# Optimization experiments

Hardware: AMD Instinct MI355X
Metric: run time of the kernel (lower is better)

The kernel has to match this reference:

```python
import jax, jax.numpy as jnp
from jax import lax
import numpy as np

B, T, IN, H = 8192, 512, 5, 32


def setup_inputs() -> dict:
    key = jax.random.key(0)
    ks = jax.random.split(key, 7)
    s_ih = 1.0 / np.sqrt(H)
    return {
        "x": jax.random.normal(ks[0], (B, T, IN), dtype=jnp.float32),
        "W_ih": jax.random.normal(ks[1], (4 * H, IN), dtype=jnp.float32) * s_ih,
        "W_hh": jax.random.normal(ks[2], (4 * H, H), dtype=jnp.float32) * s_ih,
        "b_ih": jax.random.normal(ks[3], (4 * H,), dtype=jnp.float32) * s_ih,
        "b_hh": jax.random.normal(ks[4], (4 * H,), dtype=jnp.float32) * s_ih,
        "W_fc": jax.random.normal(ks[5], (1, H), dtype=jnp.float32) * s_ih,
        "b_fc": jax.random.normal(ks[6], (1,), dtype=jnp.float32) * s_ih,
    }


def reference(x, W_ih, W_hh, b_ih, b_hh, W_fc, b_fc):
    # x: [B, T, IN]. Single-layer batch-first LSTM (PyTorch gate order i,f,g,o),
    # then linear head on the final timestep's hidden state.
    b = x.shape[0]
    h0 = jnp.zeros((b, H), x.dtype)
    c0 = jnp.zeros((b, H), x.dtype)
    # Precompute input projections for all timesteps in one GEMM: [T, B, 4H]
    x_t = jnp.swapaxes(x, 0, 1)  # [T, B, IN]
    x_proj = jnp.einsum("tbi,gi->tbg", x_t, W_ih) + b_ih + b_hh

    def step(carry, xp):
        h, c = carry
        gates = xp + h @ W_hh.T  # [B, 4H]
        i, f, g, o = jnp.split(gates, 4, axis=-1)
        i = jax.nn.sigmoid(i)
        f = jax.nn.sigmoid(f)
        g = jnp.tanh(g)
        o = jax.nn.sigmoid(o)
        c = f * c + i * g
        h = o * jnp.tanh(c)
        return (h, c), None

    (h_last, _), _ = lax.scan(step, (h0, c0), x_proj)
    return h_last @ W_fc.T + b_fc  # [B, 1]
```

## Files before the change

kernel.cpp:

```cpp
#include <hip/hip_runtime.h>


typedef __attribute__((ext_vector_type(8))) short short8;
typedef __attribute__((ext_vector_type(4))) float f32x4;
typedef __attribute__((ext_vector_type(4))) unsigned int u32x4;

static constexpr int BB  = 8192;
static constexpr int TT  = 512;
static constexpr int NIN = 5;
static constexpr int HH  = 32;

__device__ __forceinline__ unsigned short bf_rne(float f) {
    unsigned int u = __float_as_uint(f);
    u = (u + 0x7FFFu + ((u >> 16) & 1u)) >> 16;
    return (unsigned short)u;
}
__device__ __forceinline__ float bf_f32(unsigned short h) {
    return __uint_as_float((unsigned int)h << 16);
}
__device__ __forceinline__ float fast_sigmoid(float x) {
    float e = __builtin_amdgcn_exp2f(-1.4426950408889634f * x);
    return __builtin_amdgcn_rcpf(1.0f + e);
}
__device__ __forceinline__ float fast_tanh(float x) {
    float e = __builtin_amdgcn_exp2f(2.8853900817779268f * x);
    return 1.0f - 2.0f * __builtin_amdgcn_rcpf(1.0f + e);
}

__global__ __launch_bounds__(64) void lstm_wave(
    const float* __restrict__ x,
    const float* __restrict__ W_ih,
    const float* __restrict__ W_hh,
    const float* __restrict__ b_ih,
    const float* __restrict__ b_hh,
    const float* __restrict__ W_fc,
    const float* __restrict__ b_fc,
    float* __restrict__ out)
{
    const int lane = threadIdx.x & 63;
    const int col  = lane & 15;
    const int kg   = lane >> 4;
    const int b0   = blockIdx.x * 8;
    const int bloc = col & 7;
    const bool jlow = (col < 8);
    const int jbase = 4 * kg + (jlow ? 0 : 16);

    short8 Ahh_hi[8], Ahh_lo[8], Ax[8];
#pragma unroll
    for (int t4 = 0; t4 < 8; ++t4) {
        const int gr = 16 * t4 + col;
#pragma unroll
        for (int e = 0; e < 8; ++e) {
            float wv = W_hh[gr * HH + kg * 8 + e];
            unsigned short hi = bf_rne(wv);
            Ahh_hi[t4][e] = (short)hi;
            Ahh_lo[t4][e] = (short)bf_rne(wv - bf_f32(hi));
        }
        float bias = b_ih[gr] + b_hh[gr];
        unsigned short bh_ = bf_rne(bias);
        unsigned short bl_ = bf_rne(bias - bf_f32(bh_));
        short8 v;
#pragma unroll
        for (int e = 0; e < 8; ++e) v[e] = 0;
        if (kg == 0 || kg == 1) {
#pragma unroll
            for (int e = 0; e < NIN; ++e) v[e] = (short)bf_rne(W_ih[gr * NIN + e]);
            v[5] = (short)((kg == 0) ? bh_ : bl_);
        } else if (kg == 2) {
#pragma unroll
            for (int e = 0; e < NIN; ++e) {
                float wv = W_ih[gr * NIN + e];
                unsigned short h2 = bf_rne(wv);
                v[e] = (short)bf_rne(wv - bf_f32(h2));
            }
        }
        Ax[t4] = v;
    }

    const int xb = (lane / 5 < 8) ? (lane / 5) : 7;
    int xe = lane - 5 * xb; if (xe > 4) xe = 4;
    const float* px = x + ((size_t)(b0 + xb) * TT) * NIN + xe;

    const unsigned shx  = (kg == 1) ? 16u : 0u;
    const unsigned mskx = (kg == 3) ? 0u : 0xFFFFu;
    const unsigned one5 = (kg < 2) ? (0x3F80u << 16) : 0u;

    const int srcA = 32 * (kg & 1) + bloc + 8 * (kg >> 1);
    const int srcB = srcA + 16;

    float xv = px[0]; px += NIN;
    unsigned int xpk = 0;
    {
        unsigned short hi = bf_rne(xv);
        unsigned short lo = bf_rne(xv - bf_f32(hi));
        xpk = (unsigned int)hi | ((unsigned int)lo << 16);
    }

    unsigned int bh0 = 0, bh1 = 0, bh2 = 0, bh3 = 0;
    float c0 = 0.f, c1 = 0.f, c2 = 0.f, c3 = 0.f;
    float h0 = 0.f, h1 = 0.f, h2 = 0.f, h3 = 0.f;

    const f32x4 z = {0.f, 0.f, 0.f, 0.f};

#pragma unroll 1
    for (int t = 0; t < TT; ++t) {
        float xvn = xv;
        if (t + 1 < TT) { xvn = px[0]; px += NIN; }

        unsigned int p0x = (unsigned)__shfl((int)xpk, 5 * bloc + 0, 64);
        unsigned int p1x = (unsigned)__shfl((int)xpk, 5 * bloc + 1, 64);
        unsigned int p2x = (unsigned)__shfl((int)xpk, 5 * bloc + 2, 64);
        unsigned int p3x = (unsigned)__shfl((int)xpk, 5 * bloc + 3, 64);
        unsigned int p4x = (unsigned)__shfl((int)xpk, 5 * bloc + 4, 64);
        unsigned int a0 = (p0x >> shx) & mskx;
        unsigned int a1 = (p1x >> shx) & mskx;
        unsigned int a2 = (p2x >> shx) & mskx;
        unsigned int a3 = (p3x >> shx) & mskx;
        unsigned int a4 = (p4x >> shx) & mskx;
        u32x4 bxu = {a0 | (a1 << 16), a2 | (a3 << 16), a4 | one5, 0u};
        short8 bx = __builtin_bit_cast(short8, bxu);
        u32x4 bhu = {bh0, bh1, bh2, bh3};
        short8 bh = __builtin_bit_cast(short8, bhu);

        f32x4 acc[8];
#pragma unroll
        for (int t4 = 0; t4 < 8; ++t4)
            acc[t4] = __builtin_amdgcn_mfma_f32_16x16x32_bf16(Ahh_lo[t4], bh, z, 0, 0, 0);
#pragma unroll
        for (int t4 = 0; t4 < 8; ++t4)
            acc[t4] = __builtin_amdgcn_mfma_f32_16x16x32_bf16(Ahh_hi[t4], bh, acc[t4], 0, 0, 0);
#pragma unroll
        for (int t4 = 0; t4 < 8; ++t4)
            acc[t4] = __builtin_amdgcn_mfma_f32_16x16x32_bf16(Ax[t4], bx, acc[t4], 0, 0, 0);

#pragma unroll
        for (int r = 0; r < 4; ++r) {
            float gi = jlow ? acc[0][r] : acc[1][r];
            float gf = jlow ? acc[2][r] : acc[3][r];
            float gg = jlow ? acc[4][r] : acc[5][r];
            float go = jlow ? acc[6][r] : acc[7][r];
            float iv = fast_sigmoid(gi);
            float fv = fast_sigmoid(gf);
            float gv = fast_tanh(gg);
            float ov = fast_sigmoid(go);
            float cc = (r == 0 ? c0 : r == 1 ? c1 : r == 2 ? c2 : c3);
            cc = fv * cc + iv * gv;
            float hh = ov * fast_tanh(cc);
            if (r == 0) { c0 = cc; h0 = hh; }
            else if (r == 1) { c1 = cc; h1 = hh; }
            else if (r == 2) { c2 = cc; h2 = hh; }
            else { c3 = cc; h3 = hh; }
        }

        unsigned int p0 = (unsigned int)bf_rne(h0) | ((unsigned int)bf_rne(h1) << 16);
        unsigned int p1 = (unsigned int)bf_rne(h2) | ((unsigned int)bf_rne(h3) << 16);
        bh0 = (unsigned)__shfl((int)p0, srcA, 64);
        bh1 = (unsigned)__shfl((int)p1, srcA, 64);
        bh2 = (unsigned)__shfl((int)p0, srcB, 64);
        bh3 = (unsigned)__shfl((int)p1, srcB, 64);

        {
            unsigned short hi = bf_rne(xvn);
            unsigned short lo = bf_rne(xvn - bf_f32(hi));
            xpk = (unsigned int)hi | ((unsigned int)lo << 16);
        }
        xv = xvn;
    }

    float v = h0 * W_fc[jbase + 0] + h1 * W_fc[jbase + 1]
            + h2 * W_fc[jbase + 2] + h3 * W_fc[jbase + 3];
    v += __shfl_xor(v, 8);
    v += __shfl_xor(v, 16);
    v += __shfl_xor(v, 32);
    if (lane < 8) out[b0 + lane] = v + b_fc[0];
}

extern "C" void kernel_launch(void* const* d_in, const int* in_sizes, int n_in,
                              void* d_out, int out_size, void* d_ws, size_t ws_size,
                              hipStream_t stream) {
    const float* x    = (const float*)d_in[0];
    const float* W_ih = (const float*)d_in[1];
    const float* W_hh = (const float*)d_in[2];
    const float* b_ih = (const float*)d_in[3];
    const float* b_hh = (const float*)d_in[4];
    const float* W_fc = (const float*)d_in[5];
    const float* b_fc = (const float*)d_in[6];
    float* out = (float*)d_out;

    lstm_wave<<<dim3(BB / 8), dim3(64), 0, stream>>>(
        x, W_ih, W_hh, b_ih, b_hh, W_fc, b_fc, out);
}
```

Baseline: 330.2 us.

## Process four batch rows per wave to halve per-lane gate math

Each wave now handles 4 batch rows instead of 8, so every lane evaluates 2 LSTM cells per step rather than 4, and the grid doubles to 2048 waves. The shuffle mapping for the recurrent hidden state is rebuilt for the new column layout, and hardware packed bf16 conversion replaces the manual round-to-nearest code. This shortens the serial per-step activation chain. The cost is that the MFMA work per step stays the same while half of each MFMA's columns are redundant, so total matrix work doubles. A launch-bounds occupancy hint is added too.

```diff
diff --git a/kernel.cpp b/kernel.cpp
--- a/kernel.cpp
+++ b/kernel.cpp
@@ -26,8 +26,13 @@
     float e = __builtin_amdgcn_exp2f(2.8853900817779268f * x);
     return 1.0f - 2.0f * __builtin_amdgcn_rcpf(1.0f + e);
 }
-
-__global__ __launch_bounds__(64) void lstm_wave(
+__device__ __forceinline__ unsigned int cvt_pk_bf16(float a, float b) {
+    unsigned int r;
+    asm("v_cvt_pk_bf16_f32 %0, %1, %2" : "=v"(r) : "v"(a), "v"(b));
+    return r;
+}
+
+__global__ __launch_bounds__(64, 2) void lstm_wave4(
     const float* __restrict__ x,
     const float* __restrict__ W_ih,
     const float* __restrict__ W_hh,
@@ -37,13 +42,15 @@
     const float* __restrict__ b_fc,
     float* __restrict__ out)
 {
-    const int lane = threadIdx.x & 63;
-    const int col  = lane & 15;
-    const int kg   = lane >> 4;
-    const int b0   = blockIdx.x * 8;
-    const int bloc = col & 7;
-    const bool jlow = (col < 8);
-    const int jbase = 4 * kg + (jlow ? 0 : 16);
+    const int lane  = threadIdx.x & 63;
+    const int col   = lane & 15;
+    const int kg    = lane >> 4;
+    const int bloc  = col & 3;
+    const int cq    = col >> 2;
+    const int jhigh = cq >> 1;
+    const int rp    = cq & 1;
+    const int b0    = blockIdx.x * 4;
+    const int j0    = 16 * jhigh + 4 * kg + 2 * rp;
 
     short8 Ahh_hi[8], Ahh_lo[8], Ax[8];
 #pragma unroll
@@ -77,29 +84,38 @@
         Ax[t4] = v;
     }
 
-    const int xb = (lane / 5 < 8) ? (lane / 5) : 7;
+    const int xb = (lane / 5 < 4) ? (lane / 5) : 3;
     int xe = lane - 5 * xb; if (xe > 4) xe = 4;
     const float* px = x + ((size_t)(b0 + xb) * TT) * NIN + xe;
 
     const unsigned shx  = (kg == 1) ? 16u : 0u;
-    const unsigned mskx = (kg == 3) ? 0u : 0xFFFFu;
     const unsigned one5 = (kg < 2) ? (0x3F80u << 16) : 0u;
 
-    const int srcA = 32 * (kg & 1) + bloc + 8 * (kg >> 1);
-    const int srcB = srcA + 16;
+    int src0, src1, src2, src3;
+    {
+        int s[4];
+#pragma unroll
+        for (int w = 0; w < 4; ++w) {
+            const int j0s = 8 * kg + 2 * w;
+            const int jhs = j0s >> 4;
+            const int rem = j0s & 15;
+            const int kgs = rem >> 2;
+            const int rps = (rem >> 1) & 1;
+            s[w] = 16 * kgs + 4 * (2 * jhs + rps) + bloc;
+        }
+        src0 = s[0]; src1 = s[1]; src2 = s[2]; src3 = s[3];
+    }
 
     float xv = px[0]; px += NIN;
-    unsigned int xpk = 0;
+    unsigned int xpk;
     {
-        unsigned short hi = bf_rne(xv);
-        unsigned short lo = bf_rne(xv - bf_f32(hi));
-        xpk = (unsigned int)hi | ((unsigned int)lo << 16);
+        unsigned int t0 = cvt_pk_bf16(xv, xv);
+        float hif = __uint_as_float(t0 << 16);
+        xpk = cvt_pk_bf16(xv, xv - hif);
     }
 
     unsigned int bh0 = 0, bh1 = 0, bh2 = 0, bh3 = 0;
-    float c0 = 0.f, c1 = 0.f, c2 = 0.f, c3 = 0.f;
-    float h0 = 0.f, h1 = 0.f, h2 = 0.f, h3 = 0.f;
-
+    float cA = 0.f, cB = 0.f, hA = 0.f, hB = 0.f;
     const f32x4 z = {0.f, 0.f, 0.f, 0.f};
 
 #pragma unroll 1
@@ -112,11 +128,11 @@
         unsigned int p2x = (unsigned)__shfl((int)xpk, 5 * bloc + 2, 64);
         unsigned int p3x = (unsigned)__shfl((int)xpk, 5 * bloc + 3, 64);
         unsigned int p4x = (unsigned)__shfl((int)xpk, 5 * bloc + 4, 64);
-        unsigned int a0 = (p0x >> shx) & mskx;
-        unsigned int a1 = (p1x >> shx) & mskx;
-        unsigned int a2 = (p2x >> shx) & mskx;
-        unsigned int a3 = (p3x >> shx) & mskx;
-        unsigned int a4 = (p4x >> shx) & mskx;
+        unsigned int a0 = (p0x >> shx) & 0xFFFFu;
+        unsigned int a1 = (p1x >> shx) & 0xFFFFu;
+        unsigned int a2 = (p2x >> shx) & 0xFFFFu;
+        unsigned int a3 = (p3x >> shx) & 0xFFFFu;
+        unsigned int a4 = (p4x >> shx) & 0xFFFFu;
         u32x4 bxu = {a0 | (a1 << 16), a2 | (a3 << 16), a4 | one5, 0u};
         short8 bx = __builtin_bit_cast(short8, bxu);
         u32x4 bhu = {bh0, bh1, bh2, bh3};
@@ -133,46 +149,52 @@
         for (int t4 = 0; t4 < 8; ++t4)
             acc[t4] = __builtin_amdgcn_mfma_f32_16x16x32_bf16(Ax[t4], bx, acc[t4], 0, 0, 0);
 
-#pragma unroll
-        for (int r = 0; r < 4; ++r) {
-            float gi = jlow ? acc[0][r] : acc[1][r];
-            float gf = jlow ? acc[2][r] : acc[3][r];
-            float gg = jlow ? acc[4][r] : acc[5][r];
-            float go = jlow ? acc[6][r] : acc[7][r];
-            float iv = fast_sigmoid(gi);
-            float fv = fast_sigmoid(gf);
-            float gv = fast_tanh(gg);
-            float ov = fast_sigmoid(go);
-            float cc = (r == 0 ? c0 : r == 1 ? c1 : r == 2 ? c2 : c3);
-            cc = fv * cc + iv * gv;
-            float hh = ov * fast_tanh(cc);
-            if (r == 0) { c0 = cc; h0 = hh; }
-            else if (r == 1) { c1 = cc; h1 = hh; }
-            else if (r == 2) { c2 = cc; h2 = hh; }
-            else { c3 = cc; h3 = hh; }
-        }
-
-        unsigned int p0 = (unsigned int)bf_rne(h0) | ((unsigned int)bf_rne(h1) << 16);
-        unsigned int p1 = (unsigned int)bf_rne(h2) | ((unsigned int)bf_rne(h3) << 16);
-        bh0 = (unsigned)__shfl((int)p0, srcA, 64);
-        bh1 = (unsigned)__shfl((int)p1, srcA, 64);
-        bh2 = (unsigned)__shfl((int)p0, srcB, 64);
-        bh3 = (unsigned)__shfl((int)p1, srcB, 64);
+        float giA = jhigh ? (rp ? acc[1][2] : acc[1][0]) : (rp ? acc[0][2] : acc[0][0]);
+        float gfA = jhigh ? (rp ? acc[3][2] : acc[3][0]) : (rp ? acc[2][2] : acc[2][0]);
+        float ggA = jhigh ? (rp ? acc[5][2] : acc[5][0]) : (rp ? acc[4][2] : acc[4][0]);
+        float goA = jhigh ? (rp ? acc[7][2] : acc[7][0]) : (rp ? acc[6][2] : acc[6][0]);
+        float giB = jhigh ? (rp ? acc[1][3] : acc[1][1]) : (rp ? acc[0][3] : acc[0][1]);
+        float gfB = jhigh ? (rp ? acc[3][3] : acc[3][1]) : (rp ? acc[2][3] : acc[2][1]);
+        float ggB = jhigh ? (rp ? acc[5][3] : acc[5][1]) : (rp ? acc[4][3] : acc[4][1]);
+        float goB = jhigh ? (rp ? acc[7][3] : acc[7][1]) : (rp ? acc[6][3] : acc[6][1]);
 
         {
-            unsigned short hi = bf_rne(xvn);
-            unsigned short lo = bf_rne(xvn - bf_f32(hi));
-            xpk = (unsigned int)hi | ((unsigned int)lo << 16);
+            float iv = fast_sigmoid(giA);
+            float fv = fast_sigmoid(gfA);
+            float gv = fast_tanh(ggA);
+            float ov = fast_sigmoid(goA);
+            cA = fv * cA + iv * gv;
+            hA = ov * fast_tanh(cA);
+        }
+        {
+            float iv = fast_sigmoid(giB);
+            float fv = fast_sigmoid(gfB);
+            float gv = fast_tanh(ggB);
+            float ov = fast_sigmoid(goB);
+            cB = fv * cB + iv * gv;
+            hB = ov * fast_tanh(cB);
+        }
+
+        unsigned int p = cvt_pk_bf16(hA, hB);
+        bh0 = (unsigned)__shfl((int)p, src0, 64);
+        bh1 = (unsigned)__shfl((int)p, src1, 64);
+        bh2 = (unsigned)__shfl((int)p, src2, 64);
+        bh3 = (unsigned)__shfl((int)p, src3, 64);
+
+        {
+            unsigned int t0 = cvt_pk_bf16(xvn, xvn);
+            float hif = __uint_as_float(t0 << 16);
+            xpk = cvt_pk_bf16(xvn, xvn - hif);
         }
         xv = xvn;
     }
 
-    float v = h0 * W_fc[jbase + 0] + h1 * W_fc[jbase + 1]
-            + h2 * W_fc[jbase + 2] + h3 * W_fc[jbase + 3];
+    float v = hA * W_fc[j0] + hB * W_fc[j0 + 1];
+    v += __shfl_xor(v, 4);
     v += __shfl_xor(v, 8);
     v += __shfl_xor(v, 16);
     v += __shfl_xor(v, 32);
-    if (lane < 8) out[b0 + lane] = v + b_fc[0];
+    if (lane < 4) out[b0 + lane] = v + b_fc[0];
 }
 
 extern "C" void kernel_launch(void* const* d_in, const int* in_sizes, int n_in,
@@ -187,6 +209,6 @@
     const float* b_fc = (const float*)d_in[6];
     float* out = (float*)d_out;
 
-    lstm_wave<<<dim3(BB / 8), dim3(64), 0, stream>>>(
+    lstm_wave4<<<dim3(BB / 4), dim3(64), 0, stream>>>(
         x, W_ih, W_hh, b_ih, b_hh, W_fc, b_fc, out);
 }
```

Result: slower. 366.2 us (+10.9%).

## Split each wave's batch into two independent MFMA chains for ILP

Applied to the files above, without the earlier changes.

Each wave still handles 8 batch rows, but they now form two groups of 4, each with its own MFMA accumulator chain, so the two recurrences can interleave and hide MFMA and transcendental latency. The lane-to-column mapping and the hidden-state shuffle pattern are reworked so each lane owns 2 hidden units per group, which halves the per-lane gate nonlinearity work. Sigmoid pairs share one reciprocal, bf16 packing uses v_cvt_pk_bf16_f32, and each lane loads its x inputs directly instead of shuffling them. The cost is twice the MFMA count per step (16-column tiles are half empty) and higher register pressure.

```diff
diff --git a/kernel.cpp b/kernel.cpp
--- a/kernel.cpp
+++ b/kernel.cpp
@@ -9,6 +9,8 @@
 static constexpr int TT  = 512;
 static constexpr int NIN = 5;
 static constexpr int HH  = 32;
+static constexpr float K1 = 1.4426950408889634f;
+static constexpr float K2 = 2.8853900817779268f;
 
 __device__ __forceinline__ unsigned short bf_rne(float f) {
     unsigned int u = __float_as_uint(f);
@@ -18,16 +20,13 @@
 __device__ __forceinline__ float bf_f32(unsigned short h) {
     return __uint_as_float((unsigned int)h << 16);
 }
-__device__ __forceinline__ float fast_sigmoid(float x) {
-    float e = __builtin_amdgcn_exp2f(-1.4426950408889634f * x);
-    return __builtin_amdgcn_rcpf(1.0f + e);
-}
-__device__ __forceinline__ float fast_tanh(float x) {
-    float e = __builtin_amdgcn_exp2f(2.8853900817779268f * x);
-    return 1.0f - 2.0f * __builtin_amdgcn_rcpf(1.0f + e);
-}
-
-__global__ __launch_bounds__(64) void lstm_wave(
+__device__ __forceinline__ unsigned int cvt_pk_bf16(float a, float b) {
+    unsigned int r;
+    asm("v_cvt_pk_bf16_f32 %0, %1, %2" : "=v"(r) : "v"(a), "v"(b));
+    return r;
+}
+
+__global__ __launch_bounds__(64, 1) void lstm_ilp2(
     const float* __restrict__ x,
     const float* __restrict__ W_ih,
     const float* __restrict__ W_hh,
@@ -40,10 +39,12 @@
     const int lane = threadIdx.x & 63;
     const int col  = lane & 15;
     const int kg   = lane >> 4;
+    const int bloc = col & 3;
+    const int q    = col >> 2;
+    const bool jsel = (q & 1);
+    const bool rp   = (q >> 1);
     const int b0   = blockIdx.x * 8;
-    const int bloc = col & 7;
-    const bool jlow = (col < 8);
-    const int jbase = 4 * kg + (jlow ? 0 : 16);
+    const int j0   = 16 * (q & 1) + 4 * kg + 2 * (q >> 1);
 
     short8 Ahh_hi[8], Ahh_lo[8], Ax[8];
 #pragma unroll
@@ -77,102 +78,161 @@
         Ax[t4] = v;
     }
 
-    const int xb = (lane / 5 < 8) ? (lane / 5) : 7;
-    int xe = lane - 5 * xb; if (xe > 4) xe = 4;
-    const float* px = x + ((size_t)(b0 + xb) * TT) * NIN + xe;
-
-    const unsigned shx  = (kg == 1) ? 16u : 0u;
-    const unsigned mskx = (kg == 3) ? 0u : 0xFFFFu;
-    const unsigned one5 = (kg < 2) ? (0x3F80u << 16) : 0u;
-
-    const int srcA = 32 * (kg & 1) + bloc + 8 * (kg >> 1);
-    const int srcB = srcA + 16;
-
-    float xv = px[0]; px += NIN;
-    unsigned int xpk = 0;
+    int src0, src1, src2, src3;
     {
-        unsigned short hi = bf_rne(xv);
-        unsigned short lo = bf_rne(xv - bf_f32(hi));
-        xpk = (unsigned int)hi | ((unsigned int)lo << 16);
-    }
-
-    unsigned int bh0 = 0, bh1 = 0, bh2 = 0, bh3 = 0;
-    float c0 = 0.f, c1 = 0.f, c2 = 0.f, c3 = 0.f;
-    float h0 = 0.f, h1 = 0.f, h2 = 0.f, h3 = 0.f;
-
+        int s[4];
+#pragma unroll
+        for (int m = 0; m < 4; ++m) {
+            const int jw  = 8 * kg + 2 * m;
+            const int kgo = (jw & 15) >> 2;
+            const int qp  = (jw >> 4) + 2 * ((jw >> 1) & 1);
+            s[m] = 16 * kgo + 4 * qp + bloc;
+        }
+        src0 = s[0]; src1 = s[1]; src2 = s[2]; src3 = s[3];
+    }
+
+    const unsigned mskAll = (kg == 3) ? 0u : 0xFFFFFFFFu;
+    const unsigned msk45  = (kg == 3) ? 0u : ((kg == 2) ? 0x0000FFFFu : 0xFFFFFFFFu);
+    const bool isLo = (kg == 1);
+
+    const float* pA = x + (size_t)(b0 + bloc) * TT * NIN;
+    const float* pB = x + (size_t)(b0 + 4 + bloc) * TT * NIN;
+    float xA[NIN], xB[NIN];
+#pragma unroll
+    for (int e = 0; e < NIN; ++e) { xA[e] = pA[e]; xB[e] = pB[e]; }
+
+    unsigned int bhA0 = 0, bhA1 = 0, bhA2 = 0, bhA3 = 0;
+    unsigned int bhB0 = 0, bhB1 = 0, bhB2 = 0, bhB3 = 0;
+    float cA0 = 0.f, cA1 = 0.f, cB0 = 0.f, cB1 = 0.f;
+    float hA0 = 0.f, hA1 = 0.f, hB0 = 0.f, hB1 = 0.f;
     const f32x4 z = {0.f, 0.f, 0.f, 0.f};
+
+    auto make_bx = [&](const float* xv) -> short8 {
+        unsigned H01 = cvt_pk_bf16(xv[0], xv[1]);
+        unsigned H23 = cvt_pk_bf16(xv[2], xv[3]);
+        unsigned H45 = cvt_pk_bf16(xv[4], 1.0f);
+        float l0 = xv[0] - __uint_as_float(H01 << 16);
+        float l1 = xv[1] - __uint_as_float(H01 & 0xFFFF0000u);
+        float l2 = xv[2] - __uint_as_float(H23 << 16);
+        float l3 = xv[3] - __uint_as_float(H23 & 0xFFFF0000u);
+        float l4 = xv[4] - __uint_as_float(H45 << 16);
+        unsigned L01 = cvt_pk_bf16(l0, l1);
+        unsigned L23 = cvt_pk_bf16(l2, l3);
+        unsigned L45 = cvt_pk_bf16(l4, 1.0f);
+        unsigned w0 = (isLo ? L01 : H01) & mskAll;
+        unsigned w1 = (isLo ? L23 : H23) & mskAll;
+        unsigned w2 = (isLo ? L45 : H45) & msk45;
+        u32x4 u = {w0, w1, w2, 0u};
+        return __builtin_bit_cast(short8, u);
+    };
+
+    auto cell = [&](float gi, float gf, float gg, float go, float& c) -> float {
+        float ea = __builtin_amdgcn_exp2f(-K1 * gi);
+        float eb = __builtin_amdgcn_exp2f(-K1 * gf);
+        float u = 1.f + ea, v = 1.f + eb;
+        float r = __builtin_amdgcn_rcpf(u * v);
+        float iv = v * r, fv = u * r;
+        float eg = __builtin_amdgcn_exp2f(K2 * gg);
+        float eo = __builtin_amdgcn_exp2f(-K1 * go);
+        float u2 = 1.f + eg, v2 = 1.f + eo;
+        float r2 = __builtin_amdgcn_rcpf(u2 * v2);
+        float gv = 1.f - 2.f * (v2 * r2);
+        float ov = u2 * r2;
+        c = fmaf(fv, c, iv * gv);
+        float et = __builtin_amdgcn_exp2f(K2 * c);
+        float tc = 1.f - 2.f * __builtin_amdgcn_rcpf(1.f + et);
+        return ov * tc;
+    };
 
 #pragma unroll 1
     for (int t = 0; t < TT; ++t) {
-        float xvn = xv;
-        if (t + 1 < TT) { xvn = px[0]; px += NIN; }
-
-        unsigned int p0x = (unsigned)__shfl((int)xpk, 5 * bloc + 0, 64);
-        unsigned int p1x = (unsigned)__shfl((int)xpk, 5 * bloc + 1, 64);
-        unsigned int p2x = (unsigned)__shfl((int)xpk, 5 * bloc + 2, 64);
-        unsigned int p3x = (unsigned)__shfl((int)xpk, 5 * bloc + 3, 64);
-        unsigned int p4x = (unsigned)__shfl((int)xpk, 5 * bloc + 4, 64);
-        unsigned int a0 = (p0x >> shx) & mskx;
-        unsigned int a1 = (p1x >> shx) & mskx;
-        unsigned int a2 = (p2x >> shx) & mskx;
-        unsigned int a3 = (p3x >> shx) & mskx;
-        unsigned int a4 = (p4x >> shx) & mskx;
-        u32x4 bxu = {a0 | (a1 << 16), a2 | (a3 << 16), a4 | one5, 0u};
-        short8 bx = __builtin_bit_cast(short8, bxu);
-        u32x4 bhu = {bh0, bh1, bh2, bh3};
-        short8 bh = __builtin_bit_cast(short8, bhu);
-
-        f32x4 acc[8];
-#pragma unroll
-        for (int t4 = 0; t4 < 8; ++t4)
-            acc[t4] = __builtin_amdgcn_mfma_f32_16x16x32_bf16(Ahh_lo[t4], bh, z, 0, 0, 0);
-#pragma unroll
-        for (int t4 = 0; t4 < 8; ++t4)
-            acc[t4] = __builtin_amdgcn_mfma_f32_16x16x32_bf16(Ahh_hi[t4], bh, acc[t4], 0, 0, 0);
-#pragma unroll
-        for (int t4 = 0; t4 < 8; ++t4)
-            acc[t4] = __builtin_amdgcn_mfma_f32_16x16x32_bf16(Ax[t4], bx, acc[t4], 0, 0, 0);
-
-#pragma unroll
-        for (int r = 0; r < 4; ++r) {
-            float gi = jlow ? acc[0][r] : acc[1][r];
-            float gf = jlow ? acc[2][r] : acc[3][r];
-            float gg = jlow ? acc[4][r] : acc[5][r];
-            float go = jlow ? acc[6][r] : acc[7][r];
-            float iv = fast_sigmoid(gi);
-            float fv = fast_sigmoid(gf);
-            float gv = fast_tanh(gg);
-            float ov = fast_sigmoid(go);
-            float cc = (r == 0 ? c0 : r == 1 ? c1 : r == 2 ? c2 : c3);
-            cc = fv * cc + iv * gv;
-            float hh = ov * fast_tanh(cc);
-            if (r == 0) { c0 = cc; h0 = hh; }
-            else if (r == 1) { c1 = cc; h1 = hh; }
-            else if (r == 2) { c2 = cc; h2 = hh; }
-            else { c3 = cc; h3 = hh; }
-        }
-
-        unsigned int p0 = (unsigned int)bf_rne(h0) | ((unsigned int)bf_rne(h1) << 16);
-        unsigned int p1 = (unsigned int)bf_rne(h2) | ((unsigned int)bf_rne(h3) << 16);
-        bh0 = (unsigned)__shfl((int)p0, srcA, 64);
-        bh1 = (unsigned)__shfl((int)p1, srcA, 64);
-        bh2 = (unsigned)__shfl((int)p0, srcB, 64);
-        bh3 = (unsigned)__shfl((int)p1, srcB, 64);
+        const size_t off = (size_t)((t + 1 < TT) ? (t + 1) : t) * NIN;
+        float nA[NIN], nB[NIN];
+#pragma unroll
+        for (int e = 0; e < NIN; ++e) { nA[e] = pA[off + e]; nB[e] = pB[off + e]; }
+
+        short8 bxA = make_bx(xA);
+        short8 bxB = make_bx(xB);
+        u32x4 ua = {bhA0, bhA1, bhA2, bhA3};
+        u32x4 ub = {bhB0, bhB1, bhB2, bhB3};
+        short8 bhA = __builtin_bit_cast(short8, ua);
+        short8 bhB = __builtin_bit_cast(short8, ub);
+
+        f32x4 aA[8], aB[8];
+#pragma unroll
+        for (int t4 = 0; t4 < 8; ++t4) {
+            aA[t4] = __builtin_amdgcn_mfma_f32_16x16x32_bf16(Ahh_lo[t4], bhA, z, 0, 0, 0);
+            aB[t4] = __builtin_amdgcn_mfma_f32_16x16x32_bf16(Ahh_lo[t4], bhB, z, 0, 0, 0);
+        }
+#pragma unroll
+        for (int t4 = 0; t4 < 8; ++t4) {
+            aA[t4] = __builtin_amdgcn_mfma_f32_16x16x32_bf16(Ahh_hi[t4], bhA, aA[t4], 0, 0, 0);
+            aB[t4] = __builtin_amdgcn_mfma_f32_16x16x32_bf16(Ahh_hi[t4], bhB, aB[t4], 0, 0, 0);
+        }
+#pragma unroll
+        for (int t4 = 0; t4 < 8; ++t4) {
+            aA[t4] = __builtin_amdgcn_mfma_f32_16x16x32_bf16(Ax[t4], bxA, aA[t4], 0, 0, 0);
+            aB[t4] = __builtin_amdgcn_mfma_f32_16x16x32_bf16(Ax[t4], bxB, aB[t4], 0, 0, 0);
+        }
 
         {
-            unsigned short hi = bf_rne(xvn);
-            unsigned short lo = bf_rne(xvn - bf_f32(hi));
-            xpk = (unsigned int)hi | ((unsigned int)lo << 16);
-        }
-        xv = xvn;
-    }
-
-    float v = h0 * W_fc[jbase + 0] + h1 * W_fc[jbase + 1]
-            + h2 * W_fc[jbase + 2] + h3 * W_fc[jbase + 3];
-    v += __shfl_xor(v, 8);
-    v += __shfl_xor(v, 16);
-    v += __shfl_xor(v, 32);
-    if (lane < 8) out[b0 + lane] = v + b_fc[0];
+            float g[4][2];
+#pragma unroll
+            for (int G = 0; G < 4; ++G) {
+                f32x4 tA = aA[2 * G], tB = aA[2 * G + 1];
+                float s0 = jsel ? tB[0] : tA[0];
+                float s1 = jsel ? tB[1] : tA[1];
+                float s2 = jsel ? tB[2] : tA[2];
+                float s3 = jsel ? tB[3] : tA[3];
+                g[G][0] = rp ? s2 : s0;
+                g[G][1] = rp ? s3 : s1;
+            }
+            hA0 = cell(g[0][0], g[1][0], g[2][0], g[3][0], cA0);
+            hA1 = cell(g[0][1], g[1][1], g[2][1], g[3][1], cA1);
+        }
+        {
+            float g[4][2];
+#pragma unroll
+            for (int G = 0; G < 4; ++G) {
+                f32x4 tA = aB[2 * G], tB = aB[2 * G + 1];
+                float s0 = jsel ? tB[0] : tA[0];
+                float s1 = jsel ? tB[1] : tA[1];
+                float s2 = jsel ? tB[2] : tA[2];
+                float s3 = jsel ? tB[3] : tA[3];
+                g[G][0] = rp ? s2 : s0;
+                g[G][1] = rp ? s3 : s1;
+            }
+            hB0 = cell(g[0][0], g[1][0], g[2][0], g[3][0], cB0);
+            hB1 = cell(g[0][1], g[1][1], g[2][1], g[3][1], cB1);
+        }
+
+        unsigned int pkA = cvt_pk_bf16(hA0, hA1);
+        unsigned int pkB = cvt_pk_bf16(hB0, hB1);
+        bhA0 = (unsigned)__shfl((int)pkA, src0, 64);
+        bhA1 = (unsigned)__shfl((int)pkA, src1, 64);
+        bhA2 = (unsigned)__shfl((int)pkA, src2, 64);
+        bhA3 = (unsigned)__shfl((int)pkA, src3, 64);
+        bhB0 = (unsigned)__shfl((int)pkB, src0, 64);
+        bhB1 = (unsigned)__shfl((int)pkB, src1, 64);
+        bhB2 = (unsigned)__shfl((int)pkB, src2, 64);
+        bhB3 = (unsigned)__shfl((int)pkB, src3, 64);
+
+#pragma unroll
+        for (int e = 0; e < NIN; ++e) { xA[e] = nA[e]; xB[e] = nB[e]; }
+    }
+
+    const float w0 = W_fc[j0], w1 = W_fc[j0 + 1];
+    float vA = hA0 * w0 + hA1 * w1;
+    float vB = hB0 * w0 + hB1 * w1;
+    vA += __shfl_xor(vA, 4);  vB += __shfl_xor(vB, 4);
+    vA += __shfl_xor(vA, 8);  vB += __shfl_xor(vB, 8);
+    vA += __shfl_xor(vA, 16); vB += __shfl_xor(vB, 16);
+    vA += __shfl_xor(vA, 32); vB += __shfl_xor(vB, 32);
+    if (lane < 4) {
+        const float bias = b_fc[0];
+        out[b0 + lane]     = vA + bias;
+        out[b0 + 4 + lane] = vB + bias;
+    }
 }
 
 extern "C" void kernel_launch(void* const* d_in, const int* in_sizes, int n_in,
@@ -187,6 +247,6 @@
     const float* b_fc = (const float*)d_in[6];
     float* out = (float*)d_out;
 
-    lstm_wave<<<dim3(BB / 8), dim3(64), 0, stream>>>(
+    lstm_ilp2<<<dim3(BB / 8), dim3(64), 0, stream>>>(
         x, W_ih, W_hh, b_ih, b_hh, W_fc, b_fc, out);
 }
```

Measured after the change: 493.9 us. 1.5x slower.

## Replace exp-based activations with clamped Padé tanh and shared reciprocals

Applied to the files above, without the earlier changes.

Swaps the exp2/rcp sigmoid and tanh for a clamped rational (Padé) tanh approximation, writing sigmoid as 0.5+0.5*tanh(x/2). It batches the four gate denominators, and the four cell-tanh denominators, so each group shares a single reciprocal, moving work from transcendental units to FMAs. It also drops the per-step shuffles of x: each lane loads its row's five inputs directly and packs them with hardware v_cvt_pk_bf16 conversions, which also replace the manual bf16 rounding of h. Risks include accuracy loss from the clamp at ±3.5 and the polynomial approximation, extra VALU instructions, and possible overflow when four denominators are multiplied together.

```diff
diff --git a/kernel.cpp b/kernel.cpp
--- a/kernel.cpp
+++ b/kernel.cpp
@@ -18,16 +18,21 @@
 __device__ __forceinline__ float bf_f32(unsigned short h) {
     return __uint_as_float((unsigned int)h << 16);
 }
-__device__ __forceinline__ float fast_sigmoid(float x) {
-    float e = __builtin_amdgcn_exp2f(-1.4426950408889634f * x);
-    return __builtin_amdgcn_rcpf(1.0f + e);
-}
-__device__ __forceinline__ float fast_tanh(float x) {
-    float e = __builtin_amdgcn_exp2f(2.8853900817779268f * x);
-    return 1.0f - 2.0f * __builtin_amdgcn_rcpf(1.0f + e);
-}
-
-__global__ __launch_bounds__(64) void lstm_wave(
+__device__ __forceinline__ unsigned int cvt_pk_bf16(float a, float b) {
+    unsigned int r;
+    asm("v_cvt_pk_bf16_f32 %0, %1, %2" : "=v"(r) : "v"(a), "v"(b));
+    return r;
+}
+__device__ __forceinline__ void tpoly(float y, float& num, float& den) {
+    float t = y * y;
+    num = y * fmaf(t + 105.f, t, 945.f);
+    den = fmaf(fmaf(15.f, t, 420.f), t, 945.f);
+}
+__device__ __forceinline__ float clamp35(float v) {
+    return fminf(fmaxf(v, -3.5f), 3.5f);
+}
+
+__global__ __launch_bounds__(64, 1) void lstm_poly(
     const float* __restrict__ x,
     const float* __restrict__ W_ih,
     const float* __restrict__ W_hh,
@@ -77,47 +82,42 @@
         Ax[t4] = v;
     }
 
-    const int xb = (lane / 5 < 8) ? (lane / 5) : 7;
-    int xe = lane - 5 * xb; if (xe > 4) xe = 4;
-    const float* px = x + ((size_t)(b0 + xb) * TT) * NIN + xe;
-
-    const unsigned shx  = (kg == 1) ? 16u : 0u;
-    const unsigned mskx = (kg == 3) ? 0u : 0xFFFFu;
-    const unsigned one5 = (kg < 2) ? (0x3F80u << 16) : 0u;
+    const bool isLo = (kg == 1);
+    const unsigned mA  = (kg == 3) ? 0u : 0xFFFFFFFFu;
+    const unsigned m45 = (kg == 3) ? 0u : ((kg == 2) ? 0x0000FFFFu : 0xFFFFFFFFu);
 
     const int srcA = 32 * (kg & 1) + bloc + 8 * (kg >> 1);
     const int srcB = srcA + 16;
 
-    float xv = px[0]; px += NIN;
-    unsigned int xpk = 0;
-    {
-        unsigned short hi = bf_rne(xv);
-        unsigned short lo = bf_rne(xv - bf_f32(hi));
-        xpk = (unsigned int)hi | ((unsigned int)lo << 16);
-    }
+    const float* px = x + (size_t)(b0 + bloc) * TT * NIN;
+    float x0 = px[0], x1 = px[1], x2 = px[2], x3 = px[3], x4 = px[4];
 
     unsigned int bh0 = 0, bh1 = 0, bh2 = 0, bh3 = 0;
     float c0 = 0.f, c1 = 0.f, c2 = 0.f, c3 = 0.f;
     float h0 = 0.f, h1 = 0.f, h2 = 0.f, h3 = 0.f;
-
     const f32x4 z = {0.f, 0.f, 0.f, 0.f};
 
 #pragma unroll 1
     for (int t = 0; t < TT; ++t) {
-        float xvn = xv;
-        if (t + 1 < TT) { xvn = px[0]; px += NIN; }
-
-        unsigned int p0x = (unsigned)__shfl((int)xpk, 5 * bloc + 0, 64);
-        unsigned int p1x = (unsigned)__shfl((int)xpk, 5 * bloc + 1, 64);
-        unsigned int p2x = (unsigned)__shfl((int)xpk, 5 * bloc + 2, 64);
-        unsigned int p3x = (unsigned)__shfl((int)xpk, 5 * bloc + 3, 64);
-        unsigned int p4x = (unsigned)__shfl((int)xpk, 5 * bloc + 4, 64);
-        unsigned int a0 = (p0x >> shx) & mskx;
-        unsigned int a1 = (p1x >> shx) & mskx;
-        unsigned int a2 = (p2x >> shx) & mskx;
-        unsigned int a3 = (p3x >> shx) & mskx;
-        unsigned int a4 = (p4x >> shx) & mskx;
-        u32x4 bxu = {a0 | (a1 << 16), a2 | (a3 << 16), a4 | one5, 0u};
+        const size_t off = (size_t)((t + 1 < TT) ? (t + 1) : t) * NIN;
+        float n0 = px[off + 0], n1 = px[off + 1], n2 = px[off + 2],
+              n3 = px[off + 3], n4 = px[off + 4];
+
+        unsigned H01 = cvt_pk_bf16(x0, x1);
+        unsigned H23 = cvt_pk_bf16(x2, x3);
+        unsigned H45 = cvt_pk_bf16(x4, 1.0f);
+        float l0 = x0 - __uint_as_float(H01 << 16);
+        float l1 = x1 - __uint_as_float(H01 & 0xFFFF0000u);
+        float l2 = x2 - __uint_as_float(H23 << 16);
+        float l3 = x3 - __uint_as_float(H23 & 0xFFFF0000u);
+        float l4 = x4 - __uint_as_float(H45 << 16);
+        unsigned L01 = cvt_pk_bf16(l0, l1);
+        unsigned L23 = cvt_pk_bf16(l2, l3);
+        unsigned L45 = cvt_pk_bf16(l4, 1.0f);
+        unsigned w0 = (isLo ? L01 : H01) & mA;
+        unsigned w1 = (isLo ? L23 : H23) & mA;
+        unsigned w2 = (isLo ? L45 : H45) & m45;
+        u32x4 bxu = {w0, w1, w2, 0u};
         short8 bx = __builtin_bit_cast(short8, bxu);
         u32x4 bhu = {bh0, bh1, bh2, bh3};
         short8 bh = __builtin_bit_cast(short8, bhu);
@@ -133,38 +133,60 @@
         for (int t4 = 0; t4 < 8; ++t4)
             acc[t4] = __builtin_amdgcn_mfma_f32_16x16x32_bf16(Ax[t4], bx, acc[t4], 0, 0, 0);
 
+        float nc[4], dc[4], so[4];
 #pragma unroll
         for (int r = 0; r < 4; ++r) {
             float gi = jlow ? acc[0][r] : acc[1][r];
             float gf = jlow ? acc[2][r] : acc[3][r];
             float gg = jlow ? acc[4][r] : acc[5][r];
             float go = jlow ? acc[6][r] : acc[7][r];
-            float iv = fast_sigmoid(gi);
-            float fv = fast_sigmoid(gf);
-            float gv = fast_tanh(gg);
-            float ov = fast_sigmoid(go);
+
+            float yi = clamp35(gi * 0.5f);
+            float yf = clamp35(gf * 0.5f);
+            float yo = clamp35(go * 0.5f);
+            float yg = clamp35(gg);
+
+            float ni, di, nf, df, ng, dg, no, dq;
+            tpoly(yi, ni, di);
+            tpoly(yf, nf, df);
+            tpoly(yg, ng, dg);
+            tpoly(yo, no, dq);
+
+            float p01 = di * df, p23 = dg * dq;
+            float rr = __builtin_amdgcn_rcpf(p01 * p23);
+            float Ti = ni * ((df * p23) * rr);
+            float Tf = nf * ((di * p23) * rr);
+            float Tg = ng * ((p01 * dq) * rr);
+            float To = no * ((p01 * dg) * rr);
+
+            float si = fmaf(0.5f, Ti, 0.5f);
+            float sf = fmaf(0.5f, Tf, 0.5f);
+            so[r]    = fmaf(0.5f, To, 0.5f);
+
             float cc = (r == 0 ? c0 : r == 1 ? c1 : r == 2 ? c2 : c3);
-            cc = fv * cc + iv * gv;
-            float hh = ov * fast_tanh(cc);
-            if (r == 0) { c0 = cc; h0 = hh; }
-            else if (r == 1) { c1 = cc; h1 = hh; }
-            else if (r == 2) { c2 = cc; h2 = hh; }
-            else { c3 = cc; h3 = hh; }
-        }
-
-        unsigned int p0 = (unsigned int)bf_rne(h0) | ((unsigned int)bf_rne(h1) << 16);
-        unsigned int p1 = (unsigned int)bf_rne(h2) | ((unsigned int)bf_rne(h3) << 16);
+            cc = fmaf(sf, cc, si * Tg);
+            if (r == 0) c0 = cc; else if (r == 1) c1 = cc;
+            else if (r == 2) c2 = cc; else c3 = cc;
+
+            tpoly(clamp35(cc), nc[r], dc[r]);
+        }
+        {
+            float q01 = dc[0] * dc[1], q23 = dc[2] * dc[3];
+            float rr = __builtin_amdgcn_rcpf(q01 * q23);
+            h0 = so[0] * (nc[0] * ((dc[1] * q23) * rr));
+            h1 = so[1] * (nc[1] * ((dc[0] * q23) * rr));
+            h2 = so[2] * (nc[2] * ((q01 * dc[3]) * rr));
+            h3 = so[3] * (nc[3] * ((q01 * dc[2]) * rr));
+        }
+
+        unsigned int p0 = cvt_pk_bf16(h0, h1);
+        unsigned int p1 = cvt_pk_bf16(h2, h3);
         bh0 = (unsigned)__shfl((int)p0, srcA, 64);
         bh1 = (unsigned)__shfl((int)p1, srcA, 64);
         bh2 = (unsigned)__shfl((int)p0, srcB, 64);
         bh3 = (unsigned)__shfl((int)p1, srcB, 64);
 
-        {
-            unsigned short hi = bf_rne(xvn);
-            unsigned short lo = bf_rne(xvn - bf_f32(hi));
-            xpk = (unsigned int)hi | ((unsigned int)lo << 16);
-        }
-        xv = xvn;
+        x0 = n0; x1 = n1; x2 = n2; x3 = n3; x4 = n4;
     }
 
     float v = h0 * W_fc[jbase + 0] + h1 * W_fc[jbase + 1]
@@ -187,6 +209,6 @@
     const float* b_fc = (const float*)d_in[6];
     float* out = (float*)d_out;
 
-    lstm_wave<<<dim3(BB / 8), dim3(64), 0, stream>>>(
+    lstm_poly<<<dim3(BB / 8), dim3(64), 0, stream>>>(
         x, W_ih, W_hh, b_ih, b_hh, W_fc, b_fc, out);
 }
```

New measurement: 411.4 us. 1.25x slower.
